# Kernel tuning notes

Hardware: AMD Instinct MI355X
Metric: run time of the kernel (lower is better)

The kernel has to match this reference:

```python
import jax, jax.numpy as jnp
import numpy as np

VOCAB = 2048   # vocabSize; LSTM units == vocabSize in predefined_model
EMB = 256      # embDim
LAT = 16       # latDim
MAXLEN = 8     # max_senLen
PAD = 0        # PAD token (mask_zero=True masks token 0)
BATCH = 16


def lstm_lm(tokens, E, Wk, Wr, b):
    """Keras predefined_model: Embedding(mask_zero=True) -> LSTM(VOCAB) -> softmax.
    tokens: (B, T) int32. Returns (B, VOCAB) softmax of last unmasked hidden state.
    """
    x = E[tokens]                      # (B, T, EMB)
    mask = tokens != PAD               # (B, T); masked steps leave state unchanged
    B = tokens.shape[0]
    U = Wr.shape[0]
    h0 = jnp.zeros((B, U), dtype=x.dtype)
    c0 = jnp.zeros((B, U), dtype=x.dtype)

    def step(carry, inp):
        h, c = carry
        xt, m = inp                    # xt: (B, EMB), m: (B,)
        z = xt @ Wk + h @ Wr + b       # (B, 4U); Keras gate order i,f,g,o
        i, f, g, o = jnp.split(z, 4, axis=-1)
        cn = jax.nn.sigmoid(f) * c + jax.nn.sigmoid(i) * jnp.tanh(g)
        hn = jax.nn.sigmoid(o) * jnp.tanh(cn)
        m = m[:, None]
        return (jnp.where(m, hn, h), jnp.where(m, cn, c)), None

    (h, _), _ = jax.lax.scan(step, (h0, c0),
                             (jnp.swapaxes(x, 0, 1), jnp.swapaxes(mask, 0, 1)))
    return jax.nn.softmax(h, axis=-1)


def setup_inputs() -> dict:
    key = jax.random.key(0)
    k0, k1, k2, k3 = jax.random.split(key, 4)
    return {
        "input_point": jax.random.uniform(k0, (BATCH, LAT), dtype=jnp.float32),
        "E": jax.random.normal(k1, (VOCAB, EMB), dtype=jnp.float32) * 0.02,
        "Wk": jax.random.normal(k2, (EMB, 4 * VOCAB), dtype=jnp.float32) * 0.02,
        "Wr": jax.random.normal(k3, (VOCAB, 4 * VOCAB), dtype=jnp.float32) * 0.02,
        "b": jnp.zeros((4 * VOCAB,), dtype=jnp.float32),
    }


def reference(input_point, E, Wk, Wr, b):
    """Unrolls the DAriEL decoder cell over MAXLEN steps (as the wrapping RNN does).
    Per step: cond-select softmax/unfolding point, pzToSymbolAndZ (cumsum interval
    search + arithmetic-decode rescale), column scatter into tokens, LM on prefix.
    """
    B = input_point.shape[0]
    tokens = jnp.zeros((B, MAXLEN), dtype=jnp.int32)
    pad_seq = jnp.full((B, 1), PAD, dtype=jnp.int32)
    initial_softmax = lstm_lm(pad_seq, E, Wk, Wr, b)   # fully masked -> uniform
    one_softmax = initial_softmax
    unfolding = input_point
    curDim = 0
    outputs = []
    for t in range(MAXLEN):
        if t > 0:  # tf.cond(timeStep > 0, ...) exactly as written in the cell
            unfolding = input_point
            one_softmax = initial_softmax
        # pzToSymbolAndZ: locate which softmax interval contains the point
        cums = jnp.cumsum(one_softmax, axis=-1)          # (B, V) inclusive
        cums_ex = cums - one_softmax                     # exclusive cumsum
        v = unfolding[:, curDim:curDim + 1]              # (B, 1)
        inside = (cums_ex <= v) & (v <= cums)
        token = jnp.argmax(inside, axis=-1)              # (B,)
        c_lo = jnp.take_along_axis(cums_ex, token[:, None], axis=-1)
        c_hi = jnp.take_along_axis(cums, token[:, None], axis=-1)
        new_v = (v - c_lo) / (c_hi - c_lo)               # rescale into [0,1)
        unfolding = unfolding.at[:, curDim].set(new_v[:, 0])
        # replace_column(tokens, token, timeStep)
        tokens = tokens.at[:, t].set(token.astype(jnp.int32))
        # LM on decoded prefix tokens[:, :t+1]
        one_softmax = lstm_lm(tokens[:, :t + 1], E, Wk, Wr, b)
        curDim = 0 if curDim + 1 >= LAT else curDim + 1
        outputs.append(one_softmax)
    return jnp.stack(outputs, axis=1)  # (B, MAXLEN, VOCAB)
```

## Files before the change

### kernel.cpp

```cpp
#include <hip/hip_runtime.h>
#include <hip/hip_bf16.h>
#include <math.h>

#define VOCAB 2048
#define EMB 256
#define MAXLEN 8
#define NBATCH 16
#define LAT 16

typedef unsigned short u16;
typedef unsigned int u32;
using bf16x8 = __attribute__((ext_vector_type(8))) short;
using f32x4  = __attribute__((ext_vector_type(4))) float;

__device__ __forceinline__ int token_of(float v) {
    float u = v * 2048.0f;
    if (!(u >= 0.0f) || u > 2048.0f) return 0;
    int k = (int)ceilf(u) - 1;
    return k < 0 ? 0 : k;
}

__device__ __forceinline__ float sigmoidf_(float x) { return 1.0f / (1.0f + expf(-x)); }

__device__ __forceinline__ u16 to_bf16(float x) {
    __hip_bfloat16 hb = __float2bfloat16(x);
    return *reinterpret_cast<u16*>(&hb);
}


__global__ __launch_bounds__(256) void k_pack(
        const float* __restrict__ Wr, const float* __restrict__ Wk,
        const float* __restrict__ ip, const float* __restrict__ E,
        u16* __restrict__ BW, u16* __restrict__ BWk, u16* __restrict__ XA) {
    __shared__ __align__(16) u16 lds[32][128];
    int bx = blockIdx.x;
    int tid = threadIdx.x;
    if (bx < 4608) {
        const float* W; u16* dst; int kc, uc, nk0;
        if (bx < 4096) { W = Wr; dst = BW;  kc = bx >> 6;          uc = bx & 63; nk0 = 64; }
        else           { W = Wk; dst = BWk; kc = (bx - 4096) >> 6; uc = (bx - 4096) & 63; nk0 = 8; }

        #pragma unroll
        for (int it = 0; it < 2; ++it) {
            int lin = it * 256 + tid;
            int r = lin >> 4;
            int grp = lin & 15;
            const float* base = W + (size_t)(kc * 32 + r) * 8192 + uc * 32 + grp * 2;
            float2 v0 = *(const float2*)(base + 0 * 2048);
            float2 v1 = *(const float2*)(base + 1 * 2048);
            float2 v2 = *(const float2*)(base + 2 * 2048);
            float2 v3 = *(const float2*)(base + 3 * 2048);
            u16 o[8] = {to_bf16(v0.x), to_bf16(v1.x), to_bf16(v2.x), to_bf16(v3.x),
                        to_bf16(v0.y), to_bf16(v1.y), to_bf16(v2.y), to_bf16(v3.y)};
            *(uint4*)&lds[r][grp * 8] = *(uint4*)o;
        }
        __syncthreads();

        int w = tid >> 6, l = tid & 63;
        #pragma unroll
        for (int q = 0; q < 2; ++q) {
            int nt_l = q * 4 + w;
            u16 o[8];
            #pragma unroll
            for (int i = 0; i < 8; ++i) o[i] = lds[8 * (l >> 4) + i][nt_l * 16 + (l & 15)];
            int nt = uc * 8 + nt_l;
            *(uint4*)(dst + ((size_t)(nt * nk0 + kc) * 64 + l) * 8) = *(uint4*)o;
        }
    } else {
        int gidx = (bx - 4608) * 256 + tid;
        int l = gidx & 63;
        int k0 = (gidx >> 6) & 7;
        int t = gidx >> 9;
        int b = l & 15;
        int tok = token_of(ip[b * LAT + t]);
        const float* s = E + (size_t)tok * EMB + k0 * 32 + 8 * (l >> 4);
        u16 o[8];
        #pragma unroll
        for (int i = 0; i < 8; ++i) o[i] = to_bf16(s[i]);
        *(uint4*)(XA + (size_t)gidx * 8) = *(uint4*)o;
    }
}

__global__ __launch_bounds__(256) void k_xzmm0(
        const u16* __restrict__ BWk, const u16* __restrict__ XA,
        const float* __restrict__ bv, const float* __restrict__ ip,
        float* __restrict__ xz, float* __restrict__ H,
        float* __restrict__ c, u16* __restrict__ hA1) {
    int j = blockIdx.x;
    int nt = (j & 7) * 64 + (j >> 3);
    int tid = threadIdx.x;
    int w = tid >> 6, l = tid & 63;
    __shared__ float zsh0[256];

    int n = l & 15;
    float bias = bv[(n & 3) * 2048 + nt * 4 + (n >> 2)];

    const bf16x8* bp = (const bf16x8*)(BWk + ((size_t)(nt * 8) * 64 + l) * 8);
    bf16x8 bw[8];
    #pragma unroll
    for (int s = 0; s < 8; ++s) bw[s] = bp[s * 64];

    #pragma unroll
    for (int q = 0; q < 2; ++q) {
        int t = w * 2 + q;
        const bf16x8* ap = (const bf16x8*)(XA + ((size_t)(t * 8) * 64 + l) * 8);
        f32x4 acc = {bias, bias, bias, bias};
        #pragma unroll
        for (int s = 0; s < 8; ++s)
            acc = __builtin_amdgcn_mfma_f32_16x16x32_bf16(ap[s * 64], bw[s], acc, 0, 0, 0);
        #pragma unroll
        for (int i = 0; i < 4; ++i) {
            int b = 4 * (l >> 4) + i;
            xz[(((size_t)t * 512 + nt) * 16 + b) * 16 + n] = acc[i];
            if (t == 0) zsh0[b * 16 + n] = acc[i];
        }
    }
    __syncthreads();

    if (tid < 64) {
        int b = tid >> 2, ul = tid & 3;
        int myu = nt * 4 + ul;
        float z0 = zsh0[b * 16 + ul * 4 + 0];
        float z2 = zsh0[b * 16 + ul * 4 + 2];
        float z3 = zsh0[b * 16 + ul * 4 + 3];
        float cn = sigmoidf_(z0) * tanhf(z2);
        float hn = sigmoidf_(z3) * tanhf(cn);
        int tok = token_of(ip[b * LAT + 0]);
        float hw = tok != 0 ? hn : 0.0f;
        float cw = tok != 0 ? cn : 0.0f;
        c[b * 2048 + myu] = cw;
        H[b * 2048 + myu] = hw;
        u16 own = to_bf16(hw);
        int pair = __shfl_xor((int)own, 1);
        if (!(ul & 1)) {
            u32 val = (u32)own | ((u32)(u16)pair << 16);
            int k0 = myu >> 5, lg = (myu >> 3) & 3, i = myu & 7;
            *((u32*)hA1 + ((((k0 * 64) + lg * 16 + b) * 8 + i) >> 1)) = val;
        }
    }
}

__global__ __launch_bounds__(512) void k_step(
        const u16* __restrict__ BW,
        const u16* __restrict__ hAin, u16* __restrict__ hAout,
        const float* __restrict__ xz, const float* __restrict__ ip,
        float* __restrict__ c, float* __restrict__ H, int t) {
    int j = blockIdx.x;
    int nt = (j & 7) * 64 + (j >> 3);
    int tid = threadIdx.x;
    int kq = tid >> 6, l = tid & 63;
    __shared__ float zsh[8][256];

    const bf16x8* ap = (const bf16x8*)(hAin + ((size_t)(kq * 8) * 64 + l) * 8);
    const bf16x8* bp = (const bf16x8*)(BW + (((size_t)(nt * 64) + kq * 8) * 64 + l) * 8);
    bf16x8 ar[8], br[8];
    #pragma unroll
    for (int i = 0; i < 8; ++i) { ar[i] = ap[i * 64]; br[i] = bp[i * 64]; }

    f32x4 acc = {0.f, 0.f, 0.f, 0.f};
    #pragma unroll
    for (int s = 0; s < 8; ++s)
        acc = __builtin_amdgcn_mfma_f32_16x16x32_bf16(ar[s], br[s], acc, 0, 0, 0);

    #pragma unroll
    for (int i = 0; i < 4; ++i)
        zsh[kq][(4 * (l >> 4) + i) * 16 + (l & 15)] = acc[i];
    __syncthreads();

    if (tid < 64) {
        int b = tid >> 2, ul = tid & 3;
        int myu = nt * 4 + ul;
        float4 xv = *(const float4*)&xz[(((size_t)t * 512 + nt) * 16 + b) * 16 + ul * 4];
        float z[4] = {xv.x, xv.y, xv.z, xv.w};
        #pragma unroll
        for (int kk = 0; kk < 8; ++kk) {
            float4 zv = *(const float4*)&zsh[kk][b * 16 + ul * 4];
            z[0] += zv.x; z[1] += zv.y; z[2] += zv.z; z[3] += zv.w;
        }
        int idx = b * 2048 + myu;
        float co = c[idx];
        float ho = H[((size_t)(t - 1) * 16 + b) * 2048 + myu];
        float cn = sigmoidf_(z[1]) * co + sigmoidf_(z[0]) * tanhf(z[2]);
        float hn = sigmoidf_(z[3]) * tanhf(cn);
        int tok = token_of(ip[b * LAT + t]);
        float hw = tok != 0 ? hn : ho;
        float cw = tok != 0 ? cn : co;
        c[idx] = cw;
        H[((size_t)t * 16 + b) * 2048 + myu] = hw;
        u16 own = to_bf16(hw);
        int pair = __shfl_xor((int)own, 1);
        if (!(ul & 1)) {
            u32 val = (u32)own | ((u32)(u16)pair << 16);
            int k0 = myu >> 5, lg = (myu >> 3) & 3, i = myu & 7;
            *((u32*)hAout + ((((k0 * 64) + lg * 16 + b) * 8 + i) >> 1)) = val;
        }
    }
}

__global__ __launch_bounds__(256) void k_softmax(const float* __restrict__ H,
                                                 float* __restrict__ out) {
    int r = blockIdx.x;
    int t = r >> 4, b = r & 15;
    int tid = threadIdx.x;
    const float* hr = H + (size_t)r * VOCAB;
    float v[8];
    float m = -1e30f;
    #pragma unroll
    for (int i = 0; i < 8; ++i) { v[i] = hr[tid + i * 256]; m = fmaxf(m, v[i]); }

    __shared__ float redm[4], reds[4];
    int wid = tid >> 6, lane = tid & 63;
    #pragma unroll
    for (int off = 32; off; off >>= 1) m = fmaxf(m, __shfl_down(m, off));
    if (lane == 0) redm[wid] = m;
    __syncthreads();
    m = fmaxf(fmaxf(redm[0], redm[1]), fmaxf(redm[2], redm[3]));

    float e[8];
    float s = 0.0f;
    #pragma unroll
    for (int i = 0; i < 8; ++i) { e[i] = expf(v[i] - m); s += e[i]; }
    #pragma unroll
    for (int off = 32; off; off >>= 1) s += __shfl_down(s, off);
    if (lane == 0) reds[wid] = s;
    __syncthreads();
    s = reds[0] + reds[1] + reds[2] + reds[3];

    float* o = out + ((size_t)b * MAXLEN + t) * VOCAB;
    #pragma unroll
    for (int i = 0; i < 8; ++i) o[tid + i * 256] = e[i] / s;
}

extern "C" void kernel_launch(void* const* d_in, const int* in_sizes, int n_in,
                              void* d_out, int out_size, void* d_ws, size_t ws_size,
                              hipStream_t stream) {
    const float* ip = (const float*)d_in[0];
    const float* E  = (const float*)d_in[1];
    const float* Wk = (const float*)d_in[2];
    const float* Wr = (const float*)d_in[3];
    const float* bv = (const float*)d_in[4];

    char* w = (char*)d_ws;
    float* xz  = (float*)w;  w += (size_t)8 * 512 * 16 * 16 * 4;
    float* H   = (float*)w;  w += (size_t)262144 * 4;
    float* c   = (float*)w;  w += (size_t)32768 * 4;
    u16* XA  = (u16*)w;      w += (size_t)32768 * 2;
    u16* hA0 = (u16*)w;      w += (size_t)32768 * 2;
    u16* hA1 = (u16*)w;      w += (size_t)32768 * 2;
    u16* BWk = (u16*)w;      w += (size_t)2097152 * 2;
    u16* BW  = (u16*)w;      w += (size_t)16777216 * 2;

    k_pack<<<4624, 256, 0, stream>>>(Wr, Wk, ip, E, BW, BWk, XA);
    k_xzmm0<<<512, 256, 0, stream>>>(BWk, XA, bv, ip, xz, H, c, hA1);
    u16* hAbuf[2] = {hA0, hA1};
    for (int t = 1; t < MAXLEN; ++t)
        k_step<<<512, 512, 0, stream>>>(BW, hAbuf[t & 1], hAbuf[(t + 1) & 1],
                                        xz, ip, c, H, t);
    k_softmax<<<128, 256, 0, stream>>>(H, (float*)d_out);
}
```

Measured before the change: 69.94 us.

## Fuse Wk packing and input-projection GEMM into a single front kernel

Merges the pack and xz-matmul kernels into one launch. The first 512 blocks convert Wk and gather and convert embedding rows directly into registers and LDS, then run the input projection and the step-0 cell. This removes the intermediate BWk and XA buffers and one launch boundary. The remaining blocks pack Wr using float4 loads and an XOR-swizzled LDS layout to cut bank conflicts. The cost is uneven block work within a single grid.

```diff
diff --git a/kernel.cpp b/kernel.cpp
--- a/kernel.cpp
+++ b/kernel.cpp
@@ -28,31 +28,110 @@
 }
 
 
-__global__ __launch_bounds__(256) void k_pack(
+__global__ __launch_bounds__(256) void k_front(
         const float* __restrict__ Wr, const float* __restrict__ Wk,
         const float* __restrict__ ip, const float* __restrict__ E,
-        u16* __restrict__ BW, u16* __restrict__ BWk, u16* __restrict__ XA) {
-    __shared__ __align__(16) u16 lds[32][128];
+        const float* __restrict__ bv, u16* __restrict__ BW,
+        float* __restrict__ xz, float* __restrict__ H,
+        float* __restrict__ c, u16* __restrict__ hA1) {
+    __shared__ __align__(16) char smem[10240];
     int bx = blockIdx.x;
     int tid = threadIdx.x;
-    if (bx < 4608) {
-        const float* W; u16* dst; int kc, uc, nk0;
-        if (bx < 4096) { W = Wr; dst = BW;  kc = bx >> 6;          uc = bx & 63; nk0 = 64; }
-        else           { W = Wk; dst = BWk; kc = (bx - 4096) >> 6; uc = (bx - 4096) & 63; nk0 = 8; }
-
-        #pragma unroll
-        for (int it = 0; it < 2; ++it) {
+
+    if (bx < 512) {
+        u16 (*wk)[18] = (u16(*)[18])smem;
+        float* zsh0 = (float*)(smem + 9216);
+        int nt = (bx & 7) * 64 + (bx >> 3);
+        int w = tid >> 6, l = tid & 63;
+
+        #pragma unroll
+        for (int it = 0; it < 4; ++it) {
             int lin = it * 256 + tid;
-            int r = lin >> 4;
-            int grp = lin & 15;
-            const float* base = W + (size_t)(kc * 32 + r) * 8192 + uc * 32 + grp * 2;
-            float2 v0 = *(const float2*)(base + 0 * 2048);
-            float2 v1 = *(const float2*)(base + 1 * 2048);
-            float2 v2 = *(const float2*)(base + 2 * 2048);
-            float2 v3 = *(const float2*)(base + 3 * 2048);
-            u16 o[8] = {to_bf16(v0.x), to_bf16(v1.x), to_bf16(v2.x), to_bf16(v3.x),
-                        to_bf16(v0.y), to_bf16(v1.y), to_bf16(v2.y), to_bf16(v3.y)};
-            *(uint4*)&lds[r][grp * 8] = *(uint4*)o;
+            int k = lin >> 2;
+            int g = lin & 3;
+            float4 v = *(const float4*)&Wk[(size_t)k * 8192 + g * 2048 + nt * 4];
+            wk[k][0 * 4 + g] = to_bf16(v.x);
+            wk[k][1 * 4 + g] = to_bf16(v.y);
+            wk[k][2 * 4 + g] = to_bf16(v.z);
+            wk[k][3 * 4 + g] = to_bf16(v.w);
+        }
+        __syncthreads();
+
+        int n = l & 15;
+        float bias = bv[(n & 3) * 2048 + nt * 4 + (n >> 2)];
+
+        bf16x8 bw[8];
+        #pragma unroll
+        for (int s = 0; s < 8; ++s) {
+            u16 o[8];
+            #pragma unroll
+            for (int i = 0; i < 8; ++i) o[i] = wk[s * 32 + 8 * (l >> 4) + i][n];
+            bw[s] = *(bf16x8*)o;
+        }
+
+        #pragma unroll
+        for (int q = 0; q < 2; ++q) {
+            int t = w * 2 + q;
+            int tok = token_of(ip[n * LAT + t]);
+            const float* er = E + (size_t)tok * EMB + 8 * (l >> 4);
+            f32x4 acc = {bias, bias, bias, bias};
+            #pragma unroll
+            for (int s = 0; s < 8; ++s) {
+                float4 e0 = *(const float4*)(er + s * 32);
+                float4 e1 = *(const float4*)(er + s * 32 + 4);
+                u16 o[8] = {to_bf16(e0.x), to_bf16(e0.y), to_bf16(e0.z), to_bf16(e0.w),
+                            to_bf16(e1.x), to_bf16(e1.y), to_bf16(e1.z), to_bf16(e1.w)};
+                acc = __builtin_amdgcn_mfma_f32_16x16x32_bf16(*(bf16x8*)o, bw[s], acc, 0, 0, 0);
+            }
+            #pragma unroll
+            for (int i = 0; i < 4; ++i) {
+                int b = 4 * (l >> 4) + i;
+                xz[(((size_t)t * 512 + nt) * 16 + b) * 16 + n] = acc[i];
+                if (t == 0) zsh0[b * 16 + n] = acc[i];
+            }
+        }
+        __syncthreads();
+
+        if (tid < 64) {
+            int b = tid >> 2, ul = tid & 3;
+            int myu = nt * 4 + ul;
+            float z0 = zsh0[b * 16 + ul * 4 + 0];
+            float z2 = zsh0[b * 16 + ul * 4 + 2];
+            float z3 = zsh0[b * 16 + ul * 4 + 3];
+            float cn = sigmoidf_(z0) * tanhf(z2);
+            float hn = sigmoidf_(z3) * tanhf(cn);
+            int tok = token_of(ip[b * LAT + 0]);
+            float hw = tok != 0 ? hn : 0.0f;
+            float cw = tok != 0 ? cn : 0.0f;
+            c[b * 2048 + myu] = cw;
+            H[b * 2048 + myu] = hw;
+            u16 own = to_bf16(hw);
+            int pair = __shfl_xor((int)own, 1);
+            if (!(ul & 1)) {
+                u32 val = (u32)own | ((u32)(u16)pair << 16);
+                int k0 = myu >> 5, lg = (myu >> 3) & 3, i = myu & 7;
+                *((u32*)hA1 + ((((k0 * 64) + lg * 16 + b) * 8 + i) >> 1)) = val;
+            }
+        }
+    } else {
+        int pb = bx - 512;
+        int kc = pb >> 6, uc = pb & 63;
+
+        {
+            int r = tid >> 3, q8 = tid & 7;
+            const float* base = Wr + (size_t)(kc * 32 + r) * 8192 + uc * 32 + q8 * 4;
+            float4 v0 = *(const float4*)(base + 0 * 2048);
+            float4 v1 = *(const float4*)(base + 1 * 2048);
+            float4 v2 = *(const float4*)(base + 2 * 2048);
+            float4 v3 = *(const float4*)(base + 3 * 2048);
+            u16 lo[8] = {to_bf16(v0.x), to_bf16(v1.x), to_bf16(v2.x), to_bf16(v3.x),
+                         to_bf16(v0.y), to_bf16(v1.y), to_bf16(v2.y), to_bf16(v3.y)};
+            u16 hi[8] = {to_bf16(v0.z), to_bf16(v1.z), to_bf16(v2.z), to_bf16(v3.z),
+                         to_bf16(v0.w), to_bf16(v1.w), to_bf16(v2.w), to_bf16(v3.w)};
+            int key = ((r >> 3) & 3) << 5;
+            char* lp = smem + r * 256;
+            *(uint4*)(lp + ((q8 * 32) ^ key))      = *(uint4*)lo;
+            *(uint4*)(lp + ((q8 * 32 + 16) ^ key)) = *(uint4*)hi;
         }
         __syncthreads();
 
@@ -62,80 +141,13 @@
             int nt_l = q * 4 + w;
             u16 o[8];
             #pragma unroll
-            for (int i = 0; i < 8; ++i) o[i] = lds[8 * (l >> 4) + i][nt_l * 16 + (l & 15)];
+            for (int i = 0; i < 8; ++i) {
+                int rr = 8 * (l >> 4) + i;
+                int key = ((rr >> 3) & 3) << 5;
+                o[i] = *(const u16*)(smem + rr * 256 + ((nt_l * 32 + (l & 15) * 2) ^ key));
+            }
             int nt = uc * 8 + nt_l;
-            *(uint4*)(dst + ((size_t)(nt * nk0 + kc) * 64 + l) * 8) = *(uint4*)o;
-        }
-    } else {
-        int gidx = (bx - 4608) * 256 + tid;
-        int l = gidx & 63;
-        int k0 = (gidx >> 6) & 7;
-        int t = gidx >> 9;
-        int b = l & 15;
-        int tok = token_of(ip[b * LAT + t]);
-        const float* s = E + (size_t)tok * EMB + k0 * 32 + 8 * (l >> 4);
-        u16 o[8];
-        #pragma unroll
-        for (int i = 0; i < 8; ++i) o[i] = to_bf16(s[i]);
-        *(uint4*)(XA + (size_t)gidx * 8) = *(uint4*)o;
-    }
-}
-
-__global__ __launch_bounds__(256) void k_xzmm0(
-        const u16* __restrict__ BWk, const u16* __restrict__ XA,
-        const float* __restrict__ bv, const float* __restrict__ ip,
-        float* __restrict__ xz, float* __restrict__ H,
-        float* __restrict__ c, u16* __restrict__ hA1) {
-    int j = blockIdx.x;
-    int nt = (j & 7) * 64 + (j >> 3);
-    int tid = threadIdx.x;
-    int w = tid >> 6, l = tid & 63;
-    __shared__ float zsh0[256];
-
-    int n = l & 15;
-    float bias = bv[(n & 3) * 2048 + nt * 4 + (n >> 2)];
-
-    const bf16x8* bp = (const bf16x8*)(BWk + ((size_t)(nt * 8) * 64 + l) * 8);
-    bf16x8 bw[8];
-    #pragma unroll
-    for (int s = 0; s < 8; ++s) bw[s] = bp[s * 64];
-
-    #pragma unroll
-    for (int q = 0; q < 2; ++q) {
-        int t = w * 2 + q;
-        const bf16x8* ap = (const bf16x8*)(XA + ((size_t)(t * 8) * 64 + l) * 8);
-        f32x4 acc = {bias, bias, bias, bias};
-        #pragma unroll
-        for (int s = 0; s < 8; ++s)
-            acc = __builtin_amdgcn_mfma_f32_16x16x32_bf16(ap[s * 64], bw[s], acc, 0, 0, 0);
-        #pragma unroll
-        for (int i = 0; i < 4; ++i) {
-            int b = 4 * (l >> 4) + i;
-            xz[(((size_t)t * 512 + nt) * 16 + b) * 16 + n] = acc[i];
-            if (t == 0) zsh0[b * 16 + n] = acc[i];
-        }
-    }
-    __syncthreads();
-
-    if (tid < 64) {
-        int b = tid >> 2, ul = tid & 3;
-        int myu = nt * 4 + ul;
-        float z0 = zsh0[b * 16 + ul * 4 + 0];
-        float z2 = zsh0[b * 16 + ul * 4 + 2];
-        float z3 = zsh0[b * 16 + ul * 4 + 3];
-        float cn = sigmoidf_(z0) * tanhf(z2);
-        float hn = sigmoidf_(z3) * tanhf(cn);
-        int tok = token_of(ip[b * LAT + 0]);
-        float hw = tok != 0 ? hn : 0.0f;
-        float cw = tok != 0 ? cn : 0.0f;
-        c[b * 2048 + myu] = cw;
-        H[b * 2048 + myu] = hw;
-        u16 own = to_bf16(hw);
-        int pair = __shfl_xor((int)own, 1);
-        if (!(ul & 1)) {
-            u32 val = (u32)own | ((u32)(u16)pair << 16);
-            int k0 = myu >> 5, lg = (myu >> 3) & 3, i = myu & 7;
-            *((u32*)hA1 + ((((k0 * 64) + lg * 16 + b) * 8 + i) >> 1)) = val;
+            *(uint4*)(BW + ((size_t)(nt * 64 + kc) * 64 + l) * 8) = *(uint4*)o;
         }
     }
 }
@@ -244,14 +256,11 @@
     float* xz  = (float*)w;  w += (size_t)8 * 512 * 16 * 16 * 4;
     float* H   = (float*)w;  w += (size_t)262144 * 4;
     float* c   = (float*)w;  w += (size_t)32768 * 4;
-    u16* XA  = (u16*)w;      w += (size_t)32768 * 2;
     u16* hA0 = (u16*)w;      w += (size_t)32768 * 2;
     u16* hA1 = (u16*)w;      w += (size_t)32768 * 2;
-    u16* BWk = (u16*)w;      w += (size_t)2097152 * 2;
     u16* BW  = (u16*)w;      w += (size_t)16777216 * 2;
 
-    k_pack<<<4624, 256, 0, stream>>>(Wr, Wk, ip, E, BW, BWk, XA);
-    k_xzmm0<<<512, 256, 0, stream>>>(BWk, XA, bv, ip, xz, H, c, hA1);
+    k_front<<<4608, 256, 0, stream>>>(Wr, Wk, ip, E, bv, BW, xz, H, c, hA1);
     u16* hAbuf[2] = {hA0, hA1};
     for (int t = 1; t < MAXLEN; ++t)
         k_step<<<512, 512, 0, stream>>>(BW, hAbuf[t & 1], hAbuf[(t + 1) & 1],
```

After: 72.59 us. +3.8%, slower.

## Fuse step-0 input projection into pack kernel and per-step projection into k_step

Applied to the files above, without the earlier changes.

Removes the separate k_xzmm0 launch and the xz buffer. Extra blocks in k_pack read Wk and E directly to compute step 0's LSTM cell. Each k_step computes its own input projection with one extra MFMA per wave from the packed XA and BWk, so the precomputed xz activations never go through global memory. This saves a launch and roughly 2 MB of xz traffic, at the cost of one extra MFMA and two extra loads per wave on each step.

```diff
diff --git a/kernel.cpp b/kernel.cpp
--- a/kernel.cpp
+++ b/kernel.cpp
@@ -31,11 +31,14 @@
 __global__ __launch_bounds__(256) void k_pack(
         const float* __restrict__ Wr, const float* __restrict__ Wk,
         const float* __restrict__ ip, const float* __restrict__ E,
-        u16* __restrict__ BW, u16* __restrict__ BWk, u16* __restrict__ XA) {
-    __shared__ __align__(16) u16 lds[32][128];
+        const float* __restrict__ bv,
+        u16* __restrict__ BW, u16* __restrict__ BWk, u16* __restrict__ XA,
+        float* __restrict__ H, float* __restrict__ c, u16* __restrict__ hA1) {
+    __shared__ __align__(16) char smem[13312];
     int bx = blockIdx.x;
     int tid = threadIdx.x;
     if (bx < 4608) {
+        u16 (*lds)[128] = (u16(*)[128])smem;
         const float* W; u16* dst; int kc, uc, nk0;
         if (bx < 4096) { W = Wr; dst = BW;  kc = bx >> 6;          uc = bx & 63; nk0 = 64; }
         else           { W = Wk; dst = BWk; kc = (bx - 4096) >> 6; uc = (bx - 4096) & 63; nk0 = 8; }
@@ -66,7 +69,7 @@
             int nt = uc * 8 + nt_l;
             *(uint4*)(dst + ((size_t)(nt * nk0 + kc) * 64 + l) * 8) = *(uint4*)o;
         }
-    } else {
+    } else if (bx < 4624) {
         int gidx = (bx - 4608) * 256 + tid;
         int l = gidx & 63;
         int k0 = (gidx >> 6) & 7;
@@ -78,73 +81,84 @@
         #pragma unroll
         for (int i = 0; i < 8; ++i) o[i] = to_bf16(s[i]);
         *(uint4*)(XA + (size_t)gidx * 8) = *(uint4*)o;
+    } else {
+        int sb = bx - 4624;
+        int nt = (sb & 7) * 64 + (sb >> 3);
+        u16 (*wk)[18] = (u16(*)[18])smem;
+        float (*zsh0)[256] = (float(*)[256])(smem + 9216);
+        int w = tid >> 6, l = tid & 63;
+
+        #pragma unroll
+        for (int it = 0; it < 4; ++it) {
+            int lin = it * 256 + tid;
+            int k = lin >> 2, g = lin & 3;
+            float4 v = *(const float4*)&Wk[(size_t)k * 8192 + g * 2048 + nt * 4];
+            wk[k][0 * 4 + g] = to_bf16(v.x);
+            wk[k][1 * 4 + g] = to_bf16(v.y);
+            wk[k][2 * 4 + g] = to_bf16(v.z);
+            wk[k][3 * 4 + g] = to_bf16(v.w);
+        }
+        __syncthreads();
+
+        int n = l & 15;
+        f32x4 acc = {0.f, 0.f, 0.f, 0.f};
+        if (w == 0) {
+            float bias = bv[(n & 3) * 2048 + nt * 4 + (n >> 2)];
+            acc[0] = bias; acc[1] = bias; acc[2] = bias; acc[3] = bias;
+        }
+        int tok = token_of(ip[n * LAT + 0]);
+        const float* er = E + (size_t)tok * EMB + 8 * (l >> 4);
+        #pragma unroll
+        for (int q = 0; q < 2; ++q) {
+            int s = w * 2 + q;
+            u16 bo[8];
+            #pragma unroll
+            for (int i = 0; i < 8; ++i) bo[i] = wk[s * 32 + 8 * (l >> 4) + i][n];
+            float4 e0 = *(const float4*)(er + s * 32);
+            float4 e1 = *(const float4*)(er + s * 32 + 4);
+            u16 ao[8] = {to_bf16(e0.x), to_bf16(e0.y), to_bf16(e0.z), to_bf16(e0.w),
+                         to_bf16(e1.x), to_bf16(e1.y), to_bf16(e1.z), to_bf16(e1.w)};
+            acc = __builtin_amdgcn_mfma_f32_16x16x32_bf16(*(bf16x8*)ao, *(bf16x8*)bo, acc, 0, 0, 0);
+        }
+        #pragma unroll
+        for (int i = 0; i < 4; ++i)
+            zsh0[w][(4 * (l >> 4) + i) * 16 + n] = acc[i];
+        __syncthreads();
+
+        if (tid < 64) {
+            int b = tid >> 2, ul = tid & 3;
+            int myu = nt * 4 + ul;
+            float z0 = 0.f, z2 = 0.f, z3 = 0.f;
+            #pragma unroll
+            for (int ww = 0; ww < 4; ++ww) {
+                z0 += zsh0[ww][b * 16 + ul * 4 + 0];
+                z2 += zsh0[ww][b * 16 + ul * 4 + 2];
+                z3 += zsh0[ww][b * 16 + ul * 4 + 3];
+            }
+            float cn = sigmoidf_(z0) * tanhf(z2);
+            float hn = sigmoidf_(z3) * tanhf(cn);
+            int tok0 = token_of(ip[b * LAT + 0]);
+            float hw = tok0 != 0 ? hn : 0.0f;
+            float cw = tok0 != 0 ? cn : 0.0f;
+            c[b * 2048 + myu] = cw;
+            H[b * 2048 + myu] = hw;
+            u16 own = to_bf16(hw);
+            int pair = __shfl_xor((int)own, 1);
+            if (!(ul & 1)) {
+                u32 val = (u32)own | ((u32)(u16)pair << 16);
+                int k0 = myu >> 5, lg = (myu >> 3) & 3, i = myu & 7;
+                *((u32*)hA1 + ((((k0 * 64) + lg * 16 + b) * 8 + i) >> 1)) = val;
+            }
+        }
     }
 }
 
-__global__ __launch_bounds__(256) void k_xzmm0(
-        const u16* __restrict__ BWk, const u16* __restrict__ XA,
-        const float* __restrict__ bv, const float* __restrict__ ip,
-        float* __restrict__ xz, float* __restrict__ H,
-        float* __restrict__ c, u16* __restrict__ hA1) {
-    int j = blockIdx.x;
-    int nt = (j & 7) * 64 + (j >> 3);
-    int tid = threadIdx.x;
-    int w = tid >> 6, l = tid & 63;
-    __shared__ float zsh0[256];
-
-    int n = l & 15;
-    float bias = bv[(n & 3) * 2048 + nt * 4 + (n >> 2)];
-
-    const bf16x8* bp = (const bf16x8*)(BWk + ((size_t)(nt * 8) * 64 + l) * 8);
-    bf16x8 bw[8];
-    #pragma unroll
-    for (int s = 0; s < 8; ++s) bw[s] = bp[s * 64];
-
-    #pragma unroll
-    for (int q = 0; q < 2; ++q) {
-        int t = w * 2 + q;
-        const bf16x8* ap = (const bf16x8*)(XA + ((size_t)(t * 8) * 64 + l) * 8);
-        f32x4 acc = {bias, bias, bias, bias};
-        #pragma unroll
-        for (int s = 0; s < 8; ++s)
-            acc = __builtin_amdgcn_mfma_f32_16x16x32_bf16(ap[s * 64], bw[s], acc, 0, 0, 0);
-        #pragma unroll
-        for (int i = 0; i < 4; ++i) {
-            int b = 4 * (l >> 4) + i;
-            xz[(((size_t)t * 512 + nt) * 16 + b) * 16 + n] = acc[i];
-            if (t == 0) zsh0[b * 16 + n] = acc[i];
-        }
-    }
-    __syncthreads();
-
-    if (tid < 64) {
-        int b = tid >> 2, ul = tid & 3;
-        int myu = nt * 4 + ul;
-        float z0 = zsh0[b * 16 + ul * 4 + 0];
-        float z2 = zsh0[b * 16 + ul * 4 + 2];
-        float z3 = zsh0[b * 16 + ul * 4 + 3];
-        float cn = sigmoidf_(z0) * tanhf(z2);
-        float hn = sigmoidf_(z3) * tanhf(cn);
-        int tok = token_of(ip[b * LAT + 0]);
-        float hw = tok != 0 ? hn : 0.0f;
-        float cw = tok != 0 ? cn : 0.0f;
-        c[b * 2048 + myu] = cw;
-        H[b * 2048 + myu] = hw;
-        u16 own = to_bf16(hw);
-        int pair = __shfl_xor((int)own, 1);
-        if (!(ul & 1)) {
-            u32 val = (u32)own | ((u32)(u16)pair << 16);
-            int k0 = myu >> 5, lg = (myu >> 3) & 3, i = myu & 7;
-            *((u32*)hA1 + ((((k0 * 64) + lg * 16 + b) * 8 + i) >> 1)) = val;
-        }
-    }
-}
-
 __global__ __launch_bounds__(512) void k_step(
-        const u16* __restrict__ BW,
+        const u16* __restrict__ BW, const u16* __restrict__ BWk,
+        const u16* __restrict__ XA, const float* __restrict__ bv,
         const u16* __restrict__ hAin, u16* __restrict__ hAout,
-        const float* __restrict__ xz, const float* __restrict__ ip,
-        float* __restrict__ c, float* __restrict__ H, int t) {
+        const float* __restrict__ ip, float* __restrict__ c,
+        float* __restrict__ H, int t) {
     int j = blockIdx.x;
     int nt = (j & 7) * 64 + (j >> 3);
     int tid = threadIdx.x;
@@ -153,11 +167,19 @@
 
     const bf16x8* ap = (const bf16x8*)(hAin + ((size_t)(kq * 8) * 64 + l) * 8);
     const bf16x8* bp = (const bf16x8*)(BW + (((size_t)(nt * 64) + kq * 8) * 64 + l) * 8);
+    bf16x8 xa = *(const bf16x8*)(XA + ((size_t)(t * 8 + kq) * 64 + l) * 8);
+    bf16x8 xb = *(const bf16x8*)(BWk + ((size_t)(nt * 8 + kq) * 64 + l) * 8);
     bf16x8 ar[8], br[8];
     #pragma unroll
     for (int i = 0; i < 8; ++i) { ar[i] = ap[i * 64]; br[i] = bp[i * 64]; }
 
     f32x4 acc = {0.f, 0.f, 0.f, 0.f};
+    if (kq == 0) {
+        int n = l & 15;
+        float bias = bv[(n & 3) * 2048 + nt * 4 + (n >> 2)];
+        acc[0] = bias; acc[1] = bias; acc[2] = bias; acc[3] = bias;
+    }
+    acc = __builtin_amdgcn_mfma_f32_16x16x32_bf16(xa, xb, acc, 0, 0, 0);
     #pragma unroll
     for (int s = 0; s < 8; ++s)
         acc = __builtin_amdgcn_mfma_f32_16x16x32_bf16(ar[s], br[s], acc, 0, 0, 0);
@@ -170,8 +192,7 @@
     if (tid < 64) {
         int b = tid >> 2, ul = tid & 3;
         int myu = nt * 4 + ul;
-        float4 xv = *(const float4*)&xz[(((size_t)t * 512 + nt) * 16 + b) * 16 + ul * 4];
-        float z[4] = {xv.x, xv.y, xv.z, xv.w};
+        float z[4] = {0.f, 0.f, 0.f, 0.f};
         #pragma unroll
         for (int kk = 0; kk < 8; ++kk) {
             float4 zv = *(const float4*)&zsh[kk][b * 16 + ul * 4];
@@ -241,7 +262,6 @@
     const float* bv = (const float*)d_in[4];
 
     char* w = (char*)d_ws;
-    float* xz  = (float*)w;  w += (size_t)8 * 512 * 16 * 16 * 4;
     float* H   = (float*)w;  w += (size_t)262144 * 4;
     float* c   = (float*)w;  w += (size_t)32768 * 4;
     u16* XA  = (u16*)w;      w += (size_t)32768 * 2;
@@ -250,11 +270,10 @@
     u16* BWk = (u16*)w;      w += (size_t)2097152 * 2;
     u16* BW  = (u16*)w;      w += (size_t)16777216 * 2;
 
-    k_pack<<<4624, 256, 0, stream>>>(Wr, Wk, ip, E, BW, BWk, XA);
-    k_xzmm0<<<512, 256, 0, stream>>>(BWk, XA, bv, ip, xz, H, c, hA1);
+    k_pack<<<5136, 256, 0, stream>>>(Wr, Wk, ip, E, bv, BW, BWk, XA, H, c, hA1);
     u16* hAbuf[2] = {hA0, hA1};
     for (int t = 1; t < MAXLEN; ++t)
-        k_step<<<512, 512, 0, stream>>>(BW, hAbuf[t & 1], hAbuf[(t + 1) & 1],
-                                        xz, ip, c, H, t);
+        k_step<<<512, 512, 0, stream>>>(BW, BWk, XA, bv, hAbuf[t & 1], hAbuf[(t + 1) & 1],
+                                        ip, c, H, t);
     k_softmax<<<128, 256, 0, stream>>>(H, (float*)d_out);
 }
```

Measured after the change: 79.65 us. 13.9% more time.
